# Optimization experiments

Measured on AMD Instinct MI355X. Metric: run time of the kernel, lower is better.

## Reference

```python
import jax, jax.numpy as jnp
import numpy as np

D_MODEL, N_HEAD, D_HEAD = 192, 12, 16
S, B, RLEN = 1024, 4, 2048
LN_EPS = 1e-12


def _xavier(key, shape):
    fan_in, fan_out = shape[0], int(np.prod(shape[1:]))
    limit = float(np.sqrt(6.0 / (fan_in + fan_out)))
    return jax.random.uniform(key, shape, jnp.float32, -limit, limit)


def setup_inputs() -> dict:
    key = jax.random.key(0)
    ks = jax.random.split(key, 12)
    inp = {
        "x": jax.random.normal(ks[0], (S, B, D_MODEL), jnp.float32),
        "r": jax.random.normal(ks[1], (RLEN, B, D_MODEL), jnp.float32),
        "mask0": jnp.zeros((S, S, B, 1), jnp.float32),
        "Wq": _xavier(ks[2], (D_MODEL, N_HEAD, D_HEAD)),
        "Wk": _xavier(ks[3], (D_MODEL, N_HEAD, D_HEAD)),
        "Wv": _xavier(ks[4], (D_MODEL, N_HEAD, D_HEAD)),
        "Wo": _xavier(ks[5], (D_MODEL, N_HEAD, D_HEAD)),
        "Wr": _xavier(ks[6], (D_MODEL, N_HEAD, D_HEAD)),
        "r_w_bias": _xavier(ks[7], (N_HEAD, D_HEAD)),
        "r_r_bias": _xavier(ks[8], (N_HEAD, D_HEAD)),
        "ln_w": jnp.ones((D_MODEL,), jnp.float32),
        "ln_b": jnp.zeros((D_MODEL,), jnp.float32),
    }
    return inp


def _rel_shift_bnij(x, klen):
    # x: [b, n, i, j] with j = rlen; XLNet relative shift, keep first klen cols
    b, n, i, j = x.shape
    x = x.reshape(b, n, j, i)[:, :, 1:, :].reshape(b, n, i, j - 1)
    return x[:, :, :, :klen]


def reference(x, r, mask0, Wq, Wk, Wv, Wo, Wr, r_w_bias, r_r_bias, ln_w, ln_b):
    mask0 = jnp.zeros_like(mask0)  # Model.forward zeroes the mask
    q_head = jnp.einsum("ibh,hnd->ibnd", x, Wq)
    k_head = jnp.einsum("ibh,hnd->ibnd", x, Wk)
    v_head = jnp.einsum("ibh,hnd->ibnd", x, Wv)
    k_head_r = jnp.einsum("ibh,hnd->ibnd", r, Wr)

    # content-based score
    ac = jnp.einsum("ibnd,jbnd->bnij", q_head + r_w_bias, k_head)
    # position-based score with relative shift
    bd = jnp.einsum("ibnd,jbnd->bnij", q_head + r_r_bias, k_head_r)
    bd = _rel_shift_bnij(bd, ac.shape[3])
    # seg_mat is None -> segment term ef = 0

    scale = 1.0 / np.sqrt(D_HEAD)
    attn_score = (ac + bd) * scale
    attn_score = attn_score - 1e30 * jnp.einsum("ijbn->bnij", mask0)
    attn_prob = jax.nn.softmax(attn_score, axis=3)

    attn_vec = jnp.einsum("bnij,jbnd->ibnd", attn_prob, v_head)
    attn_out = jnp.einsum("ibnd,hnd->ibh", attn_vec, Wo)

    out = attn_out + x  # residual
    mean = jnp.mean(out, axis=-1, keepdims=True)
    var = jnp.mean(jnp.square(out - mean), axis=-1, keepdims=True)
    out = (out - mean) * jax.lax.rsqrt(var + LN_EPS) * ln_w + ln_b
    return out
```

## Files before the change

kernel.cpp:

```cpp
#include <hip/hip_runtime.h>
#include <hip/hip_bf16.h>

#define SQ   1024
#define BB   4
#define DM   192
#define NH   12
#define DH   16
#define RL   2048
#define BN   (BB*NH)

typedef __attribute__((ext_vector_type(8))) short  short8;
typedef __attribute__((ext_vector_type(4))) float  f32x4;
typedef __attribute__((ext_vector_type(2))) float  f32x2;
typedef __attribute__((ext_vector_type(2))) unsigned u32x2;
typedef __attribute__((ext_vector_type(4))) unsigned u32x4;

__device__ __forceinline__ short f2bf(float f) {
    unsigned u = __float_as_uint(f);
    u += 0x7fff + ((u >> 16) & 1);
    return (short)(u >> 16);
}
__device__ __forceinline__ unsigned pkbf(float lo, float hi) {
    union { __hip_bfloat162 h; unsigned u; } cv;
    cv.h = __float22bfloat162_rn(make_float2(lo, hi));
    return cv.u;
}
__device__ __forceinline__ short8 as_s8(u32x4 v) {
    union { u32x4 u; short8 s; } c; c.u = v; return c.s;
}

__global__ __launch_bounds__(256) void k_prep(
    const float* __restrict__ x, const float* __restrict__ r,
    const float* __restrict__ Wq, const float* __restrict__ Wk,
    const float* __restrict__ Wv, const float* __restrict__ Wr,
    const float* __restrict__ Wo,
    unsigned short* __restrict__ xb, unsigned short* __restrict__ rb,
    unsigned short* __restrict__ WTq, unsigned short* __restrict__ WTk,
    unsigned short* __restrict__ WTv, unsigned short* __restrict__ WTr,
    unsigned short* __restrict__ Wob)
{
    int idx = blockIdx.x * 256 + threadIdx.x;
    if (idx < 786432) { xb[idx] = (unsigned short)f2bf(x[idx]); return; }
    idx -= 786432;
    if (idx < 1572864) { rb[idx] = (unsigned short)f2bf(r[idx]); return; }
    idx -= 1572864;
    if (idx < 36864) { int nd = idx / 192, h = idx % 192;
                       WTq[idx] = (unsigned short)f2bf(Wq[h*192 + nd]); return; }
    idx -= 36864;
    if (idx < 36864) { int nd = idx / 192, h = idx % 192;
                       WTk[idx] = (unsigned short)f2bf(Wk[h*192 + nd]); return; }
    idx -= 36864;
    if (idx < 36864) { int nd = idx / 192, h = idx % 192;
                       WTv[idx] = (unsigned short)f2bf(Wv[h*192 + nd]); return; }
    idx -= 36864;
    if (idx < 36864) { int nd = idx / 192, h = idx % 192;
                       WTr[idx] = (unsigned short)f2bf(Wr[h*192 + nd]); return; }
    idx -= 36864;
    if (idx < 36864) { Wob[idx] = (unsigned short)f2bf(Wo[idx]); return; }
}

__global__ __launch_bounds__(256) void k_gemm_xr(
    const unsigned short* __restrict__ xb, const unsigned short* __restrict__ rbm,
    const unsigned short* __restrict__ WTq, const unsigned short* __restrict__ WTk,
    const unsigned short* __restrict__ WTv, const unsigned short* __restrict__ WTr,
    const float* __restrict__ rwb, const float* __restrict__ rrb,
    unsigned short* __restrict__ qwb, unsigned short* __restrict__ qrb,
    unsigned short* __restrict__ kh, unsigned short* __restrict__ vh,
    unsigned short* __restrict__ kr)
{
    int bid = blockIdx.x;
    int tid = threadIdx.x, w = tid >> 6, lane = tid & 63, g = lane >> 4, mm = lane & 15;
    if (bid < 1152) {
        int rt2 = bid / 9, ch = bid % 9;
        int wsel = ch / 3, sub = ch % 3;
        int c0 = sub * 64 + w * 16;
        const unsigned short* WT = (wsel == 0) ? WTq : ((wsel == 1) ? WTk : WTv);
        const unsigned short* arow0 = xb + (size_t)(rt2*32 + mm) * 192 + 8*g;
        const unsigned short* arow1 = arow0 + 16*192;
        const unsigned short* brow = WT + (size_t)(c0 + mm) * 192 + 8*g;
        f32x4 acc0 = {0.f,0.f,0.f,0.f}, acc1 = {0.f,0.f,0.f,0.f};
        #pragma unroll
        for (int kk = 0; kk < 6; ++kk) {
            short8 b  = *(const short8*)(brow  + kk*32);
            short8 a0 = *(const short8*)(arow0 + kk*32);
            short8 a1 = *(const short8*)(arow1 + kk*32);
            acc0 = __builtin_amdgcn_mfma_f32_16x16x32_bf16(a0, b, acc0, 0, 0, 0);
            acc1 = __builtin_amdgcn_mfma_f32_16x16x32_bf16(a1, b, acc1, 0, 0, 0);
        }
        int col = c0 + mm, n = col >> 4, d = col & 15;
        if (wsel == 0) {
            const float SCL = 0.3606737602222409f;
            float bw = rwb[col], br = rrb[col];
            #pragma unroll
            for (int r = 0; r < 4; ++r) {
                int row = rt2*32 + 4*g + r;
                int i = row >> 2, b2 = row & 3;
                size_t o = ((size_t)(b2*NH + n) * SQ + i) * DH + d;
                qwb[o] = (unsigned short)f2bf((acc0[r] + bw) * SCL);
                qrb[o] = (unsigned short)f2bf((acc0[r] + br) * SCL);
                int row1 = row + 16;
                int i1 = row1 >> 2, b21 = row1 & 3;
                size_t o1 = ((size_t)(b21*NH + n) * SQ + i1) * DH + d;
                qwb[o1] = (unsigned short)f2bf((acc1[r] + bw) * SCL);
                qrb[o1] = (unsigned short)f2bf((acc1[r] + br) * SCL);
            }
        } else {
            unsigned short* dst = (wsel == 1) ? kh : vh;
            #pragma unroll
            for (int r = 0; r < 4; ++r) {
                int row = rt2*32 + 4*g + r;
                int i = row >> 2, b2 = row & 3;
                dst[((size_t)(b2*NH + n) * SQ + i) * DH + d] = (unsigned short)f2bf(acc0[r]);
                int row1 = row + 16;
                int i1 = row1 >> 2, b21 = row1 & 3;
                dst[((size_t)(b21*NH + n) * SQ + i1) * DH + d] = (unsigned short)f2bf(acc1[r]);
            }
        }
    } else {
        int bb = bid - 1152;
        int rt2 = bb / 3, sub = bb % 3;
        int c0 = sub * 64 + w * 16;
        const unsigned short* arow0 = rbm + (size_t)(rt2*32 + mm) * 192 + 8*g;
        const unsigned short* arow1 = arow0 + 16*192;
        const unsigned short* brow = WTr + (size_t)(c0 + mm) * 192 + 8*g;
        f32x4 acc0 = {0.f,0.f,0.f,0.f}, acc1 = {0.f,0.f,0.f,0.f};
        #pragma unroll
        for (int kk = 0; kk < 6; ++kk) {
            short8 b  = *(const short8*)(brow  + kk*32);
            short8 a0 = *(const short8*)(arow0 + kk*32);
            short8 a1 = *(const short8*)(arow1 + kk*32);
            acc0 = __builtin_amdgcn_mfma_f32_16x16x32_bf16(a0, b, acc0, 0, 0, 0);
            acc1 = __builtin_amdgcn_mfma_f32_16x16x32_bf16(a1, b, acc1, 0, 0, 0);
        }
        int col = c0 + mm, n = col >> 4, d = col & 15;
        #pragma unroll
        for (int r = 0; r < 4; ++r) {
            int row = rt2*32 + 4*g + r;
            int j = row >> 2, b2 = row & 3;
            kr[((size_t)(b2*NH + n) * RL + j) * DH + d] = (unsigned short)f2bf(acc0[r]);
            int row1 = row + 16;
            int j1 = row1 >> 2, b21 = row1 & 3;
            kr[((size_t)(b21*NH + n) * RL + j1) * DH + d] = (unsigned short)f2bf(acc1[r]);
        }
    }
}

__global__ __launch_bounds__(256, 3) void k_attn_mfma(
    const unsigned short* __restrict__ qwb, const unsigned short* __restrict__ qrb,
    const unsigned short* __restrict__ kh, const unsigned short* __restrict__ vh,
    const unsigned short* __restrict__ kr, unsigned short* __restrict__ av_b)
{
    __shared__ __align__(16) short vbuf[4][2][64*16];
    __shared__ __align__(16) float bdls[4][16*86];

    int bid = blockIdx.x;
    int logical = (bid & 7) * 96 + (bid >> 3);
    int bn = logical >> 4;
    int i0b = (logical & 15) * 64;
    int tid = threadIdx.x, w = tid >> 6, lane = tid & 63;
    int g = lane >> 4, mm = lane & 15;
    size_t headK = (size_t)bn * SQ * DH;
    size_t headR = (size_t)bn * RL * DH;
    int koff = 8 * (g & 1);

    short8 qwf = {0,0,0,0,0,0,0,0}, qrf = {0,0,0,0,0,0,0,0};
    if (g < 2) {
        int qrow = i0b + 16*w + mm;
        qwf = *(const short8*)((const short*)qwb + headK + (size_t)qrow*DH + 8*g);
        qrf = *(const short8*)((const short*)qrb + headK + (size_t)qrow*DH + 8*g);
    }

    {
        const unsigned short* p = vh + headK + (size_t)lane*16;
        u32x4 a0 = *(const u32x4*)p, a1 = *(const u32x4*)(p + 8);
        *(u32x4*)(&vbuf[w][0][lane*16])     = a0;
        *(u32x4*)(&vbuf[w][0][lane*16 + 8]) = a1;
    }
    const int basew0 = 1008 - i0b - 16*w;
    u32x4 ka[4], krg[5], kan[4], krn[5];
    #pragma unroll
    for (int tp = 0; tp < 4; ++tp)
        ka[tp] = *(const u32x4*)(kh + headK + (size_t)(16*tp + mm)*16 + koff);
    #pragma unroll
    for (int tau = 0; tau < 5; ++tau)
        krg[tau] = *(const u32x4*)(kr + headR + (size_t)(basew0 + 16*tau + mm)*16 + koff);

    float Lacc = 0.f;
    f32x4 opv = {0.f,0.f,0.f,0.f};
    float* bw_ = &bdls[w][0];
    const f32x4 z = {0.f,0.f,0.f,0.f};

    for (int t = 0; t < 16; ++t) {
        int cur = t & 1;
        u32x4 sva = {0,0,0,0}, svb = {0,0,0,0};
        bool ds = (t < 15);
        if (ds) {
            #pragma unroll
            for (int tp = 0; tp < 4; ++tp)
                kan[tp] = *(const u32x4*)(kh + headK + (size_t)(64*(t+1) + 16*tp + mm)*16 + koff);
            #pragma unroll
            for (int tau = 0; tau < 5; ++tau)
                krn[tau] = *(const u32x4*)(kr + headR + (size_t)(basew0 + 64*(t+1) + 16*tau + mm)*16 + koff);
            const unsigned short* p = vh + headK + (size_t)(64*(t+1) + lane)*16;
            sva = *(const u32x4*)p; svb = *(const u32x4*)(p + 8);
        }

        #pragma unroll
        for (int tau = 0; tau < 5; ++tau) {
            f32x4 bd = __builtin_amdgcn_mfma_f32_16x16x32_bf16(as_s8(krg[tau]), qrf, z, 0, 0, 0);
            int wb = mm*86 + 16*tau + 4*g;
            f32x2 lo, hi;
            lo[0] = bd[0]; lo[1] = bd[1];
            hi[0] = bd[2]; hi[1] = bd[3];
            *(f32x2*)(bw_ + wb)     = lo;
            *(f32x2*)(bw_ + wb + 2) = hi;
        }

        unsigned pk[8]; float Lc = 0.f;
        #pragma unroll
        for (int tp = 0; tp < 4; ++tp) {
            f32x4 ac = __builtin_amdgcn_mfma_f32_16x16x32_bf16(as_s8(ka[tp]), qwf, z, 0, 0, 0);
            int cb = mm*86 + 16*tp + 4*g + 16 - mm;
            float p0 = __builtin_amdgcn_exp2f(ac[0] + bw_[cb + 0]);
            float p1 = __builtin_amdgcn_exp2f(ac[1] + bw_[cb + 1]);
            float p2 = __builtin_amdgcn_exp2f(ac[2] + bw_[cb + 2]);
            float p3 = __builtin_amdgcn_exp2f(ac[3] + bw_[cb + 3]);
            Lc += (p0 + p1) + (p2 + p3);
            pk[2*tp]     = pkbf(p0, p1);
            pk[2*tp + 1] = pkbf(p2, p3);
        }
        Lacc += Lc;

        unsigned vb0 = (unsigned)(size_t)(&vbuf[w][cur][0])
                     + ((unsigned)mm << 3) + ((unsigned)g << 7);
        {
            u32x2 t0, t1;
            asm volatile("ds_read_b64_tr_b16 %0, %2 offset:0\n\t"
                         "ds_read_b64_tr_b16 %1, %2 offset:512\n\t"
                         "s_waitcnt lgkmcnt(0)"
                         : "=&v"(t0), "=&v"(t1) : "v"(vb0));
            __builtin_amdgcn_sched_barrier(0);
            union { unsigned u[4]; short8 s; } va, pb;
            va.u[0]=t0[0]; va.u[1]=t0[1]; va.u[2]=t1[0]; va.u[3]=t1[1];
            pb.u[0]=pk[0]; pb.u[1]=pk[1]; pb.u[2]=pk[2]; pb.u[3]=pk[3];
            opv = __builtin_amdgcn_mfma_f32_16x16x32_bf16(va.s, pb.s, opv, 0, 0, 0);
        }
        {
            u32x2 t0, t1;
            asm volatile("ds_read_b64_tr_b16 %0, %2 offset:1024\n\t"
                         "ds_read_b64_tr_b16 %1, %2 offset:1536\n\t"
                         "s_waitcnt lgkmcnt(0)"
                         : "=&v"(t0), "=&v"(t1) : "v"(vb0));
            __builtin_amdgcn_sched_barrier(0);
            union { unsigned u[4]; short8 s; } va, pb;
            va.u[0]=t0[0]; va.u[1]=t0[1]; va.u[2]=t1[0]; va.u[3]=t1[1];
            pb.u[0]=pk[4]; pb.u[1]=pk[5]; pb.u[2]=pk[6]; pb.u[3]=pk[7];
            opv = __builtin_amdgcn_mfma_f32_16x16x32_bf16(va.s, pb.s, opv, 0, 0, 0);
        }

        if (ds) {
            *(u32x4*)(&vbuf[w][cur^1][lane*16])     = sva;
            *(u32x4*)(&vbuf[w][cur^1][lane*16 + 8]) = svb;
            #pragma unroll
            for (int tp = 0; tp < 4; ++tp) ka[tp] = kan[tp];
            #pragma unroll
            for (int tau = 0; tau < 5; ++tau) krg[tau] = krn[tau];
        }
    }

    Lacc += __shfl_xor(Lacc, 16);
    Lacc += __shfl_xor(Lacc, 32);
    float inv = 1.0f / Lacc;
    int b2 = bn / NH, nn = bn % NH;
    int i = i0b + 16*w + mm;
    unsigned o0 = pkbf(opv[0]*inv, opv[1]*inv);
    unsigned o1 = pkbf(opv[2]*inv, opv[3]*inv);
    u32x2 ov = {o0, o1};
    *(u32x2*)(av_b + ((size_t)i*4 + b2)*192 + nn*16 + 4*g) = ov;
}

__global__ __launch_bounds__(256) void k_out_ln(
    const unsigned short* __restrict__ avb, const unsigned short* __restrict__ Wob,
    const float* __restrict__ x,
    const float* __restrict__ lnw, const float* __restrict__ lnb,
    float* __restrict__ out)
{
    __shared__ __align__(16) float os[16][196];
    int tid = threadIdx.x, w = tid >> 6, lane = tid & 63, g = lane >> 4, mm = lane & 15;
    int rt = blockIdx.x;
    const unsigned short* arow = avb + (size_t)(rt*16 + mm)*192 + 8*g;
    short8 a[6];
    #pragma unroll
    for (int kk = 0; kk < 6; ++kk) a[kk] = *(const short8*)(arow + kk*32);
    #pragma unroll
    for (int s = 0; s < 3; ++s) {
        int c0 = w*48 + s*16;
        const unsigned short* brow = Wob + (size_t)(c0 + mm)*192 + 8*g;
        f32x4 acc = {0.f,0.f,0.f,0.f};
        #pragma unroll
        for (int kk = 0; kk < 6; ++kk) {
            short8 b = *(const short8*)(brow + kk*32);
            acc = __builtin_amdgcn_mfma_f32_16x16x32_bf16(a[kk], b, acc, 0, 0, 0);
        }
        int col = c0 + mm;
        #pragma unroll
        for (int r = 0; r < 4; ++r) {
            int rl = 4*g + r;
            os[rl][col] = acc[r] + x[(size_t)(rt*16 + rl)*192 + col];
        }
    }
    __syncthreads();
    int row = tid >> 4, seg = tid & 15;
    const float* ors = &os[row][0] + seg*12;
    f32x4 v0 = *(const f32x4*)(ors);
    f32x4 v1 = *(const f32x4*)(ors + 4);
    f32x4 v2 = *(const f32x4*)(ors + 8);
    float s1 = ((v0[0]+v0[1])+(v0[2]+v0[3])) + ((v1[0]+v1[1])+(v1[2]+v1[3]))
             + ((v2[0]+v2[1])+(v2[2]+v2[3]));
    float q1 = ((v0[0]*v0[0]+v0[1]*v0[1])+(v0[2]*v0[2]+v0[3]*v0[3]))
             + ((v1[0]*v1[0]+v1[1]*v1[1])+(v1[2]*v1[2]+v1[3]*v1[3]))
             + ((v2[0]*v2[0]+v2[1]*v2[1])+(v2[2]*v2[2]+v2[3]*v2[3]));
    #pragma unroll
    for (int off = 1; off < 16; off <<= 1) {
        s1 += __shfl_xor(s1, off);
        q1 += __shfl_xor(q1, off);
    }
    float mean = s1 * (1.0f / 192.0f);
    float var  = q1 * (1.0f / 192.0f) - mean * mean;
    float rstd = rsqrtf(var + 1e-12f);
    int c0 = seg * 12;
    size_t ro = (size_t)(rt*16 + row) * 192;
    #pragma unroll
    for (int c = 0; c < 12; ++c) {
        float v = (c < 4) ? v0[c] : ((c < 8) ? v1[c-4] : v2[c-8]);
        out[ro + c0 + c] = (v - mean) * rstd * lnw[c0 + c] + lnb[c0 + c];
    }
}

extern "C" void kernel_launch(void* const* d_in, const int* in_sizes, int n_in,
                              void* d_out, int out_size, void* d_ws, size_t ws_size,
                              hipStream_t stream) {
    const float* x   = (const float*)d_in[0];
    const float* r   = (const float*)d_in[1];
    const float* Wq  = (const float*)d_in[3];
    const float* Wk  = (const float*)d_in[4];
    const float* Wv  = (const float*)d_in[5];
    const float* Wo  = (const float*)d_in[6];
    const float* Wr  = (const float*)d_in[7];
    const float* rwb = (const float*)d_in[8];
    const float* rrb = (const float*)d_in[9];
    const float* lnw = (const float*)d_in[10];
    const float* lnb = (const float*)d_in[11];
    float* out = (float*)d_out;

    char* ws = (char*)d_ws;
    unsigned short* qwb = (unsigned short*)(ws + 0);
    unsigned short* qrb = (unsigned short*)(ws + 1572864);
    unsigned short* kh  = (unsigned short*)(ws + 3145728);
    unsigned short* vh  = (unsigned short*)(ws + 4718592);
    unsigned short* kr  = (unsigned short*)(ws + 6291456);
    unsigned short* avb = (unsigned short*)(ws + 9437184);
    unsigned short* xb  = (unsigned short*)(ws + 11010048);
    unsigned short* rb  = (unsigned short*)(ws + 12582912);
    unsigned short* WTq = (unsigned short*)(ws + 15728640);
    unsigned short* WTk = (unsigned short*)(ws + 15802368);
    unsigned short* WTv = (unsigned short*)(ws + 15876096);
    unsigned short* WTr = (unsigned short*)(ws + 15949824);
    unsigned short* Wob = (unsigned short*)(ws + 16023552);

    k_prep<<<dim3(9936), dim3(256), 0, stream>>>(x, r, Wq, Wk, Wv, Wr, Wo,
                                                 xb, rb, WTq, WTk, WTv, WTr, Wob);
    k_gemm_xr<<<dim3(1920), dim3(256), 0, stream>>>(xb, rb, WTq, WTk, WTv, WTr,
                                                    rwb, rrb, qwb, qrb, kh, vh, kr);
    k_attn_mfma<<<dim3(768), dim3(256), 0, stream>>>(qwb, qrb, kh, vh, kr, avb);
    k_out_ln<<<dim3(256), dim3(256), 0, stream>>>(avb, Wob, x, lnw, lnb, out);
}
```

Before: 61.65 us.

## Split attention key range across two blocks and combine partials in output kernel

Each attention block now processes half of the key/position range, doubling the grid, and writes unnormalized fp32 partial outputs and softmax denominators. The output-projection kernel sums the two partials, normalizes, and converts to bf16 before the Wo GEMM. This aims to raise occupancy and latency hiding on the attention kernel at the cost of extra fp32 partial traffic and a shorter per-block pipeline. Workspace is reorganized so partials reuse the bf16 x/r staging buffers.

```diff
diff --git a/kernel.cpp b/kernel.cpp
--- a/kernel.cpp
+++ b/kernel.cpp
@@ -148,15 +148,18 @@
 __global__ __launch_bounds__(256, 3) void k_attn_mfma(
     const unsigned short* __restrict__ qwb, const unsigned short* __restrict__ qrb,
     const unsigned short* __restrict__ kh, const unsigned short* __restrict__ vh,
-    const unsigned short* __restrict__ kr, unsigned short* __restrict__ av_b)
+    const unsigned short* __restrict__ kr,
+    float* __restrict__ pO, float* __restrict__ pL)
 {
     __shared__ __align__(16) short vbuf[4][2][64*16];
     __shared__ __align__(16) float bdls[4][16*86];
 
     int bid = blockIdx.x;
-    int logical = (bid & 7) * 96 + (bid >> 3);
-    int bn = logical >> 4;
-    int i0b = (logical & 15) * 64;
+    int logical = (bid & 7) * 192 + (bid >> 3);
+    int h = logical & 1;
+    int l2 = logical >> 1;
+    int bn = l2 >> 4;
+    int i0b = (l2 & 15) * 64;
     int tid = threadIdx.x, w = tid >> 6, lane = tid & 63;
     int g = lane >> 4, mm = lane & 15;
     size_t headK = (size_t)bn * SQ * DH;
@@ -170,8 +173,9 @@
         qrf = *(const short8*)((const short*)qrb + headK + (size_t)qrow*DH + 8*g);
     }
 
+    const int t0 = 8*h, tEnd = 8*h + 8;
     {
-        const unsigned short* p = vh + headK + (size_t)lane*16;
+        const unsigned short* p = vh + headK + (size_t)(64*t0 + lane)*16;
         u32x4 a0 = *(const u32x4*)p, a1 = *(const u32x4*)(p + 8);
         *(u32x4*)(&vbuf[w][0][lane*16])     = a0;
         *(u32x4*)(&vbuf[w][0][lane*16 + 8]) = a1;
@@ -180,20 +184,20 @@
     u32x4 ka[4], krg[5], kan[4], krn[5];
     #pragma unroll
     for (int tp = 0; tp < 4; ++tp)
-        ka[tp] = *(const u32x4*)(kh + headK + (size_t)(16*tp + mm)*16 + koff);
+        ka[tp] = *(const u32x4*)(kh + headK + (size_t)(64*t0 + 16*tp + mm)*16 + koff);
     #pragma unroll
     for (int tau = 0; tau < 5; ++tau)
-        krg[tau] = *(const u32x4*)(kr + headR + (size_t)(basew0 + 16*tau + mm)*16 + koff);
+        krg[tau] = *(const u32x4*)(kr + headR + (size_t)(basew0 + 64*t0 + 16*tau + mm)*16 + koff);
 
     float Lacc = 0.f;
     f32x4 opv = {0.f,0.f,0.f,0.f};
     float* bw_ = &bdls[w][0];
     const f32x4 z = {0.f,0.f,0.f,0.f};
 
-    for (int t = 0; t < 16; ++t) {
+    for (int t = t0; t < tEnd; ++t) {
         int cur = t & 1;
         u32x4 sva = {0,0,0,0}, svb = {0,0,0,0};
-        bool ds = (t < 15);
+        bool ds = (t < tEnd - 1);
         if (ds) {
             #pragma unroll
             for (int tp = 0; tp < 4; ++tp)
@@ -234,26 +238,26 @@
         unsigned vb0 = (unsigned)(size_t)(&vbuf[w][cur][0])
                      + ((unsigned)mm << 3) + ((unsigned)g << 7);
         {
-            u32x2 t0, t1;
+            u32x2 t0r, t1r;
             asm volatile("ds_read_b64_tr_b16 %0, %2 offset:0\n\t"
                          "ds_read_b64_tr_b16 %1, %2 offset:512\n\t"
                          "s_waitcnt lgkmcnt(0)"
-                         : "=&v"(t0), "=&v"(t1) : "v"(vb0));
+                         : "=&v"(t0r), "=&v"(t1r) : "v"(vb0));
             __builtin_amdgcn_sched_barrier(0);
             union { unsigned u[4]; short8 s; } va, pb;
-            va.u[0]=t0[0]; va.u[1]=t0[1]; va.u[2]=t1[0]; va.u[3]=t1[1];
+            va.u[0]=t0r[0]; va.u[1]=t0r[1]; va.u[2]=t1r[0]; va.u[3]=t1r[1];
             pb.u[0]=pk[0]; pb.u[1]=pk[1]; pb.u[2]=pk[2]; pb.u[3]=pk[3];
             opv = __builtin_amdgcn_mfma_f32_16x16x32_bf16(va.s, pb.s, opv, 0, 0, 0);
         }
         {
-            u32x2 t0, t1;
+            u32x2 t0r, t1r;
             asm volatile("ds_read_b64_tr_b16 %0, %2 offset:1024\n\t"
                          "ds_read_b64_tr_b16 %1, %2 offset:1536\n\t"
                          "s_waitcnt lgkmcnt(0)"
-                         : "=&v"(t0), "=&v"(t1) : "v"(vb0));
+                         : "=&v"(t0r), "=&v"(t1r) : "v"(vb0));
             __builtin_amdgcn_sched_barrier(0);
             union { unsigned u[4]; short8 s; } va, pb;
-            va.u[0]=t0[0]; va.u[1]=t0[1]; va.u[2]=t1[0]; va.u[3]=t1[1];
+            va.u[0]=t0r[0]; va.u[1]=t0r[1]; va.u[2]=t1r[0]; va.u[3]=t1r[1];
             pb.u[0]=pk[4]; pb.u[1]=pk[5]; pb.u[2]=pk[6]; pb.u[3]=pk[7];
             opv = __builtin_amdgcn_mfma_f32_16x16x32_bf16(va.s, pb.s, opv, 0, 0, 0);
         }
@@ -270,17 +274,15 @@
 
     Lacc += __shfl_xor(Lacc, 16);
     Lacc += __shfl_xor(Lacc, 32);
-    float inv = 1.0f / Lacc;
-    int b2 = bn / NH, nn = bn % NH;
     int i = i0b + 16*w + mm;
-    unsigned o0 = pkbf(opv[0]*inv, opv[1]*inv);
-    unsigned o1 = pkbf(opv[2]*inv, opv[3]*inv);
-    u32x2 ov = {o0, o1};
-    *(u32x2*)(av_b + ((size_t)i*4 + b2)*192 + nn*16 + 4*g) = ov;
+    size_t po = ((size_t)(h*48 + bn)*1024 + i)*16 + 4*g;
+    *(f32x4*)(pO + po) = opv;
+    if (g == 0) pL[(size_t)(h*48 + bn)*1024 + i] = Lacc;
 }
 
 __global__ __launch_bounds__(256) void k_out_ln(
-    const unsigned short* __restrict__ avb, const unsigned short* __restrict__ Wob,
+    const float* __restrict__ pO, const float* __restrict__ pL,
+    const unsigned short* __restrict__ Wob,
     const float* __restrict__ x,
     const float* __restrict__ lnw, const float* __restrict__ lnb,
     float* __restrict__ out)
@@ -288,10 +290,27 @@
     __shared__ __align__(16) float os[16][196];
     int tid = threadIdx.x, w = tid >> 6, lane = tid & 63, g = lane >> 4, mm = lane & 15;
     int rt = blockIdx.x;
-    const unsigned short* arow = avb + (size_t)(rt*16 + mm)*192 + 8*g;
+    int R = rt*16 + mm, i = R >> 2, b2 = R & 3;
     short8 a[6];
     #pragma unroll
-    for (int kk = 0; kk < 6; ++kk) a[kk] = *(const short8*)(arow + kk*32);
+    for (int kk = 0; kk < 6; ++kk) {
+        int nn = 2*kk + (g >> 1);
+        int bn = b2*12 + nn;
+        size_t base0 = ((size_t)bn*1024 + i)*16 + 8*(g & 1);
+        size_t base1 = base0 + (size_t)48*1024*16;
+        f32x4 o0a = *(const f32x4*)(pO + base0);
+        f32x4 o0b = *(const f32x4*)(pO + base0 + 4);
+        f32x4 o1a = *(const f32x4*)(pO + base1);
+        f32x4 o1b = *(const f32x4*)(pO + base1 + 4);
+        float L = pL[(size_t)bn*1024 + i] + pL[(size_t)(48 + bn)*1024 + i];
+        float inv = 1.0f / L;
+        union { unsigned u[4]; short8 s; } cv;
+        cv.u[0] = pkbf((o0a[0]+o1a[0])*inv, (o0a[1]+o1a[1])*inv);
+        cv.u[1] = pkbf((o0a[2]+o1a[2])*inv, (o0a[3]+o1a[3])*inv);
+        cv.u[2] = pkbf((o0b[0]+o1b[0])*inv, (o0b[1]+o1b[1])*inv);
+        cv.u[3] = pkbf((o0b[2]+o1b[2])*inv, (o0b[3]+o1b[3])*inv);
+        a[kk] = cv.s;
+    }
     #pragma unroll
     for (int s = 0; s < 3; ++s) {
         int c0 = w*48 + s*16;
@@ -359,19 +378,20 @@
     unsigned short* kh  = (unsigned short*)(ws + 3145728);
     unsigned short* vh  = (unsigned short*)(ws + 4718592);
     unsigned short* kr  = (unsigned short*)(ws + 6291456);
-    unsigned short* avb = (unsigned short*)(ws + 9437184);
-    unsigned short* xb  = (unsigned short*)(ws + 11010048);
-    unsigned short* rb  = (unsigned short*)(ws + 12582912);
-    unsigned short* WTq = (unsigned short*)(ws + 15728640);
-    unsigned short* WTk = (unsigned short*)(ws + 15802368);
-    unsigned short* WTv = (unsigned short*)(ws + 15876096);
-    unsigned short* WTr = (unsigned short*)(ws + 15949824);
-    unsigned short* Wob = (unsigned short*)(ws + 16023552);
+    unsigned short* WTq = (unsigned short*)(ws + 9437184);
+    unsigned short* WTk = (unsigned short*)(ws + 9510912);
+    unsigned short* WTv = (unsigned short*)(ws + 9584640);
+    unsigned short* WTr = (unsigned short*)(ws + 9658368);
+    unsigned short* Wob = (unsigned short*)(ws + 9732096);
+    unsigned short* xb  = (unsigned short*)(ws + 9805824);
+    unsigned short* rb  = (unsigned short*)(ws + 11378688);
+    float*          pO  = (float*)(ws + 9805824);
+    float*          pL  = (float*)(ws + 16097280);
 
     k_prep<<<dim3(9936), dim3(256), 0, stream>>>(x, r, Wq, Wk, Wv, Wr, Wo,
                                                  xb, rb, WTq, WTk, WTv, WTr, Wob);
     k_gemm_xr<<<dim3(1920), dim3(256), 0, stream>>>(xb, rb, WTq, WTk, WTv, WTr,
                                                     rwb, rrb, qwb, qrb, kh, vh, kr);
-    k_attn_mfma<<<dim3(768), dim3(256), 0, stream>>>(qwb, qrb, kh, vh, kr, avb);
-    k_out_ln<<<dim3(256), dim3(256), 0, stream>>>(avb, Wob, x, lnw, lnb, out);
-}
+    k_attn_mfma<<<dim3(1536), dim3(256), 0, stream>>>(qwb, qrb, kh, vh, kr, pO, pL);
+    k_out_ln<<<dim3(256), dim3(256), 0, stream>>>(pO, pL, Wob, x, lnw, lnb, out);
+}
```

After: 67.50 us. 1.1x slower.
